# Optimization experiments

Measured on AMD Instinct MI355X. Metric: run time of the kernel, lower is better.

Reference implementation:

```python
import jax, jax.numpy as jnp
import numpy as np
from jax.scipy.special import erf

T_OBS = 1.0
T_CONTROL = 3.0
B = 4096
NT = 2048
DT0 = 0.002


def _moments(t_obs):
    t_avg = t_obs / 2.0
    t2_avg = t_obs ** 2 / 3.0
    C_t = t2_avg - t_avg ** 2
    return t_avg, t2_avg, C_t


def _sigma_move(sig_f, sig_a, xi_f, xi_v, t_obs):
    # 3x3 posterior covariance over (a, f, v), per get_Sigma_move_noSM
    xi_f_ = xi_f * (np.sqrt(t_obs) / sig_f)
    xi_v_ = xi_v * (np.sqrt(t_obs) / sig_f)
    t_avg, t2_avg, C_t = _moments(t_obs)
    det_inv = (1 + 1 / xi_f_ ** 2) * (C_t + 1 / xi_v_ ** 2) + t_avg ** 2 / xi_f_ ** 2
    pre = sig_f ** 2 / t_obs / det_inv ** 2
    Sff = (C_t + 1 / xi_v_ ** 2) ** 2 + C_t * t_avg ** 2
    Sfv = t_avg * (1 / (xi_f_ * xi_v_) ** 2 - C_t)
    Svv = (t_avg / xi_f_ ** 2) ** 2 + C_t * (1 + 1 / xi_f_ ** 2) ** 2
    zz = jnp.zeros(())
    row0 = jnp.stack([sig_a ** 2, zz, zz])
    row1 = jnp.stack([zz, pre * Sff, pre * Sfv])
    row2 = jnp.stack([zz, pre * Sfv, pre * Svv])
    return jnp.stack([row0, row1, row2])


def _sigma_stat(sig_f, xi_f, xi_v, t_obs):
    # 2x2 posterior covariance over (f, v), per get_Sigma_stat_noSM
    xi_f_ = xi_f * (np.sqrt(t_obs) / sig_f)
    xi_v_ = xi_v * (np.sqrt(t_obs) / sig_f)
    t_avg, t2_avg, C_t = _moments(t_obs)
    det_inv = (1 + 1 / xi_f_ ** 2) * (C_t + 1 / xi_v_ ** 2) + t_avg ** 2 / xi_f_ ** 2
    pre = sig_f ** 2 / t_obs
    Sff = pre / (1 + 1 / xi_f_ ** 2) ** 2
    Sfv = pre * (t_avg / (xi_f_ ** 2 + 1)) / det_inv
    Svv = pre * ((t_avg / xi_f_ ** 2) ** 2 + C_t * (1 + 1 / xi_f_ ** 2) ** 2) / det_inv ** 2
    return jnp.stack([jnp.stack([Sff, Sfv]), jnp.stack([Sfv, Svv])])


def _threshold(sig_f, xi_f, xi_v, d0, t_obs):
    xi_f_ = xi_f * (np.sqrt(t_obs) / sig_f)
    xi_v_ = xi_v * (np.sqrt(t_obs) / sig_f)
    t_avg, t2_avg, C_t = _moments(t_obs)
    log_arg = 1 + xi_v_ ** 2 * (C_t + t2_avg / (1 + xi_f_ ** 2))
    det_ratio = t_obs / sig_f ** 2 * (C_t + 1 / xi_v_ ** 2 + t2_avg / (1 + xi_f_ ** 2))
    thresh_sq = (jnp.log(log_arg) - 2 * d0) / det_ratio
    return jnp.sqrt(jax.nn.relu(thresh_sq))


def _control_weights(tau, t_wait, alpha, T_control):
    # Control-A gain profiles over the (shared) time grid tau [NT].
    Tm = T_control - jnp.mean(t_wait)
    rem = jax.nn.relu(Tm - tau)
    w_f = alpha * rem / Tm
    w_v = alpha * rem ** 2 / (2 * Tm ** 2)
    w_o_move = jnp.stack([w_f, w_v])          # [2, NT]
    w_o_stat = w_f[None, :]                   # [1, NT]
    w_tx = alpha * jnp.ones_like(tau)         # [NT]
    w_tv = alpha * rem / Tm                   # [NT]
    return w_o_move, w_o_stat, w_tx, w_tv


def _get_L(u_t, x_t, z, dt, Sinv_m, Sinv_s, det_m, det_s, W_m, W_s, q,
           wo_m, wo_s, w_tx, w_tv, g, sig_a):
    z_noa = z[:, 1:]
    num_t = u_t.shape[1]
    g2 = g * g
    resid = u_t - w_tx[None, :] * x_t                          # [B, T]
    data_quad = 0.5 * (dt / g2) * jnp.sum(resid ** 2, axis=-1)  # [B]

    def branch(Sinv, W, zz, wo, with_ctrl_v):
        S_vv = Sinv[-1, -1]
        S_vo = Sinv[-1, :-1]
        S_oo = Sinv[:-1, :-1]
        W_v = W[-1]
        W_o = W[:-1]
        A = S_oo[None] + (dt[:, None, None] / g2) * (wo @ wo.T)[None]  # [B,no,no]
        A_inv = jnp.linalg.inv(A)
        det_A = jnp.linalg.det(A)
        Woz = zz @ W_o.T                                       # [B, no]
        Wvz = zz @ W_v                                         # [B]
        d = (dt[:, None] / g2) * jnp.einsum('it,bt->bi', wo, resid)
        J_r = Woz @ S_oo.T + Wvz[:, None] * S_vo[None, :] + d   # [B, no]
        if with_ctrl_v:
            J_v = S_vo[None, :] + (dt[:, None] / g2) * (wo @ w_tv)[None, :]
            J = (S_vv * Wvz + Woz @ S_vo
                 + (dt / g2) * jnp.einsum('t,bt->b', w_tv, resid)
                 - jnp.einsum('bi,bij,bj->b', J_r, A_inv, J_v))
            k = (S_vv + (dt / g2) * jnp.sum(w_tv ** 2)
                 - jnp.einsum('bi,bij,bj->b', J_v, A_inv, J_v))
        else:
            J_v = jnp.broadcast_to(S_vo[None, :], J_r.shape)
            J = (S_vv * Wvz + Woz @ S_vo
                 - jnp.einsum('bi,bij,bj->b', J_r, A_inv, J_v))
            k = S_vv - jnp.einsum('bi,bij,bj->b', J_v, A_inv, J_v)
        Z = (0.5 * jnp.einsum('bi,ij,jk,kl,bl->b', zz, W, Sinv, W, zz)
             + data_quad
             - 0.5 * jnp.einsum('bi,bij,bj->b', J_r, A_inv, J_r)
             - 0.5 * J * J / k)
        return J, k, Z, det_A

    J_m, k_m, Z_m, detA_m = branch(Sinv_m, W_m, z, wo_m, True)
    J_s, k_s, Z_s, detA_s = branch(Sinv_s, W_s, z_noa, wo_s, False)

    pre_m = k_m * detA_m * det_m * sig_a ** 2
    pre_s = k_s * detA_s * det_s
    erf_m = (1 + 0.5 * erf((J_m - k_m * q) / jnp.sqrt(2 * k_m))
             - 0.5 * erf((J_m + k_m * q) / jnp.sqrt(2 * k_m)))
    erf_s = (0.5 * erf((J_s + k_s * q) / jnp.sqrt(2 * k_s))
             - 0.5 * erf((J_s - k_s * q) / jnp.sqrt(2 * k_s)))
    L_m = jnp.exp(-Z_m) * erf_m / jnp.sqrt(pre_m)
    L_s = jnp.exp(-Z_s) * erf_s / jnp.sqrt(pre_s)
    return jnp.sum(num_t * jnp.log(2 * np.pi * g2 / dt) - jnp.log(L_m + L_s))


def _forward(u_t, x_t, z, t, t_wait, u_t_SM, x_t_SM, z_SM, t_SM, t_wait_SM,
             hsig_f, hsig_w, hxi_f, hxi_w, hxi_v, delta0, halpha, hg, hW_aa, hsig_a):
    sig_f = jnp.exp(hsig_f[0]); sig_w = jnp.exp(hsig_w[0])
    xi_f = jnp.exp(hxi_f[0]); xi_w = jnp.exp(hxi_w[0]); xi_v = jnp.exp(hxi_v[0])
    d0 = delta0[0]; alpha = jnp.exp(halpha[0]); g = jnp.exp(hg[0])
    W_aa = jnp.exp(hW_aa[0]); sig_a = jnp.exp(hsig_a[0])
    one = jnp.ones(())

    dt = t[:, 1] - t[:, 0]
    dt_SM = t_SM[:, 1] - t[:, 0]  # matches original code (uses t[:,0])

    # ---- no self-motion branch ----
    Sig_m = _sigma_move(sig_f, sig_a, xi_f, xi_v, T_OBS)
    Sig_s = _sigma_stat(sig_f, xi_f, xi_v, T_OBS)
    Sinv_m = jnp.linalg.inv(Sig_m); det_m = jnp.linalg.det(Sig_m)
    Sinv_s = jnp.linalg.inv(Sig_s); det_s = jnp.linalg.det(Sig_s)
    W_m = jnp.diag(jnp.stack([W_aa, one, alpha]))
    W_s = jnp.diag(jnp.stack([one, alpha]))
    q = _threshold(sig_f, xi_f, xi_v, d0, T_OBS)
    wo_m, wo_s, w_tx, w_tv = _control_weights(t[0], t_wait, alpha, T_CONTROL)
    L1 = _get_L(u_t, x_t, z, dt, Sinv_m, Sinv_s, det_m, det_s,
                W_m, W_s, q, wo_m, wo_s, w_tx, w_tv, g, sig_a)

    # ---- self-motion branch: noise inflated by sig_w / xi_w, gain scaled by W_aa ----
    sig_eff = jnp.sqrt(sig_f ** 2 + sig_w ** 2)
    xi_v_eff = jnp.sqrt(xi_v ** 2 + xi_w ** 2)
    alpha_sm = alpha * W_aa
    Sig_m2 = _sigma_move(sig_eff, sig_a, xi_f, xi_v_eff, T_OBS)
    Sig_s2 = _sigma_stat(sig_eff, xi_f, xi_v_eff, T_OBS)
    Sinv_m2 = jnp.linalg.inv(Sig_m2); det_m2 = jnp.linalg.det(Sig_m2)
    Sinv_s2 = jnp.linalg.inv(Sig_s2); det_s2 = jnp.linalg.det(Sig_s2)
    W_m2 = jnp.diag(jnp.stack([W_aa, one, alpha_sm]))
    W_s2 = jnp.diag(jnp.stack([one, alpha_sm]))
    q2 = _threshold(sig_eff, xi_f, xi_v_eff, d0, T_OBS)
    wo_m2, wo_s2, w_tx2, w_tv2 = _control_weights(t_SM[0], t_wait_SM, alpha_sm, T_CONTROL)
    L2 = _get_L(u_t_SM, x_t_SM, z_SM, dt_SM, Sinv_m2, Sinv_s2, det_m2, det_s2,
                W_m2, W_s2, q2, wo_m2, wo_s2, w_tx2, w_tv2, g, sig_a)
    return L1 + L2


def setup_inputs() -> dict:
    key = jax.random.key(0)
    ks = jax.random.split(key, 8)
    f32 = jnp.float32
    tau = jnp.arange(NT, dtype=f32) * DT0
    t = jnp.broadcast_to(tau, (B, NT))
    return {
        'u_t': 0.05 * jax.random.normal(ks[0], (B, NT), f32),
        'x_t': 0.05 * jax.random.normal(ks[1], (B, NT), f32),
        'z': 0.1 * jax.random.normal(ks[2], (B, 3), f32),
        't': t,
        't_wait': 0.3 * jax.random.uniform(ks[3], (B,), f32),
        'u_t_SM': 0.05 * jax.random.normal(ks[4], (B, NT), f32),
        'x_t_SM': 0.05 * jax.random.normal(ks[5], (B, NT), f32),
        'z_SM': 0.1 * jax.random.normal(ks[6], (B, 3), f32),
        't_SM': t,
        't_wait_SM': 0.3 * jax.random.uniform(ks[7], (B,), f32),
        'hsig_f': jnp.array([-0.7], f32),
        'hsig_w': jnp.array([-1.0], f32),
        'hxi_f': jnp.array([0.0], f32),
        'hxi_w': jnp.array([-0.5], f32),
        'hxi_v': jnp.array([0.0], f32),
        'delta0': jnp.array([-0.5], f32),
        'halpha': jnp.array([-0.3], f32),
        'hg': jnp.array([0.0], f32),
        'hW_aa': jnp.array([-0.2], f32),
        'hsig_a': jnp.array([-0.7], f32),
    }


def reference(u_t, x_t, z, t, t_wait, u_t_SM, x_t_SM, z_SM, t_SM, t_wait_SM,
              hsig_f, hsig_w, hxi_f, hxi_w, hxi_v, delta0, halpha, hg, hW_aa, hsig_a):
    return _forward(u_t, x_t, z, t, t_wait, u_t_SM, x_t_SM, z_SM, t_SM, t_wait_SM,
                    hsig_f, hsig_w, hxi_f, hxi_w, hxi_v, delta0, halpha, hg, hW_aa, hsig_a)
```

## Files before the change

### kernel.cpp

```cpp
#include <hip/hip_runtime.h>
#include <math.h>

#ifndef M_PI
#define M_PI 3.14159265358979323846
#endif

#define TPB 256


__device__ double block_sum_d(double v, double* buf) {
    int tid = threadIdx.x;
    buf[tid] = v;
    __syncthreads();
    for (int o = TPB / 2; o > 0; o >>= 1) {
        if (tid < o) buf[tid] += buf[tid + o];
        __syncthreads();
    }
    double r = buf[0];
    __syncthreads();
    return r;
}

__global__ __launch_bounds__(TPB) void precompute_kernel(
    const float* __restrict__ t, const float* __restrict__ t_wait,
    const float* __restrict__ t_SM, const float* __restrict__ t_wait_SM,
    const float* __restrict__ hsig_f, const float* __restrict__ hsig_w,
    const float* __restrict__ hxi_f, const float* __restrict__ hxi_w,
    const float* __restrict__ hxi_v, const float* __restrict__ delta0,
    const float* __restrict__ halpha, const float* __restrict__ hg,
    const float* __restrict__ hW_aa, const float* __restrict__ hsig_a,
    int B, int NT, double* __restrict__ ws)
{
    __shared__ double buf[TPB];
    __shared__ double sh[2];
    int tid = threadIdx.x;

    double s1 = 0.0, s2 = 0.0;
    for (int i = tid; i < B; i += TPB) {
        s1 += (double)t_wait[i];
        s2 += (double)t_wait_SM[i];
    }
    double tw1 = block_sum_d(s1, buf);
    double tw2 = block_sum_d(s2, buf);
    if (tid == 0) { sh[0] = 3.0 - tw1 / (double)B; sh[1] = 3.0 - tw2 / (double)B; }
    __syncthreads();
    double Tm1 = sh[0], Tm2 = sh[1];

    double a2 = 0, a3 = 0, a4 = 0, b2 = 0, b3 = 0, b4 = 0;
    for (int i = tid; i < NT; i += TPB) {
        double r1 = Tm1 - (double)t[i];    r1 = r1 > 0.0 ? r1 : 0.0;
        double r2 = Tm2 - (double)t_SM[i]; r2 = r2 > 0.0 ? r2 : 0.0;
        double r1s = r1 * r1, r2s = r2 * r2;
        a2 += r1s; a3 += r1s * r1; a4 += r1s * r1s;
        b2 += r2s; b3 += r2s * r2; b4 += r2s * r2s;
    }
    a2 = block_sum_d(a2, buf); a3 = block_sum_d(a3, buf); a4 = block_sum_d(a4, buf);
    b2 = block_sum_d(b2, buf); b3 = block_sum_d(b3, buf); b4 = block_sum_d(b4, buf);
    if (tid != 0) return;

    double sig_f = exp((double)hsig_f[0]);
    double sig_w = exp((double)hsig_w[0]);
    double xi_f  = exp((double)hxi_f[0]);
    double xi_w  = exp((double)hxi_w[0]);
    double xi_v  = exp((double)hxi_v[0]);
    double d0    = (double)delta0[0];
    double alpha = exp((double)halpha[0]);
    double g     = exp((double)hg[0]);
    double W_aa  = exp((double)hW_aa[0]);
    double sig_a = exp((double)hsig_a[0]);
    double g2 = g * g, sig_a2 = sig_a * sig_a;

    for (int L = 0; L < 2; ++L) {
        double sf, xv, ab, Tm, S2, S3, S4;
        if (L == 0) { sf = sig_f; xv = xi_v; ab = alpha; Tm = Tm1; S2 = a2; S3 = a3; S4 = a4; }
        else {
            sf = sqrt(sig_f * sig_f + sig_w * sig_w);
            xv = sqrt(xi_v * xi_v + xi_w * xi_w);
            ab = alpha * W_aa; Tm = Tm2; S2 = b2; S3 = b3; S4 = b4;
        }
        double xf_ = xi_f / sf, xv_ = xv / sf;
        double t_avg = 0.5, t2_avg = 1.0 / 3.0, C_t = 1.0 / 12.0;
        double ixf2 = 1.0 / (xf_ * xf_), ixv2 = 1.0 / (xv_ * xv_);
        double det_inv = (1.0 + ixf2) * (C_t + ixv2) + t_avg * t_avg * ixf2;

        double pre_m = sf * sf / (det_inv * det_inv);
        double Sff = (C_t + ixv2) * (C_t + ixv2) + C_t * t_avg * t_avg;
        double Sfv = t_avg * (ixf2 * ixv2 - C_t);
        double Svv = (t_avg * ixf2) * (t_avg * ixf2) + C_t * (1.0 + ixf2) * (1.0 + ixf2);
        double m11 = pre_m * Sff, m12 = pre_m * Sfv, m22 = pre_m * Svv;
        double detB = m11 * m22 - m12 * m12;
        double Sm00 = 1.0 / sig_a2, Sm01 = 0.0, Sm02 = 0.0;
        double Sm11 = m22 / detB, Sm12 = -m12 / detB, Sm22 = m11 / detB;
        double det_m = sig_a2 * detB;

        double pre_s = sf * sf;
        double Sffs = pre_s / ((1.0 + ixf2) * (1.0 + ixf2));
        double Sfvs = pre_s * (t_avg / (xf_ * xf_ + 1.0)) / det_inv;
        double Svvs = pre_s * ((t_avg * ixf2) * (t_avg * ixf2) + C_t * (1.0 + ixf2) * (1.0 + ixf2)) / (det_inv * det_inv);
        double det_s = Sffs * Svvs - Sfvs * Sfvs;
        double Ss00 = Svvs / det_s, Ss01 = -Sfvs / det_s, Ss11 = Sffs / det_s;

        double log_arg = 1.0 + xv_ * xv_ * (C_t + t2_avg / (1.0 + xf_ * xf_));
        double det_ratio = (1.0 / (sf * sf)) * (C_t + 1.0 / (xv_ * xv_) + t2_avg / (1.0 + xf_ * xf_));
        double tq = (log(log_arg) - 2.0 * d0) / det_ratio;
        double q = sqrt(tq > 0.0 ? tq : 0.0);

        double kf = ab / Tm, kv = ab / (2.0 * Tm * Tm);
        double Gff = kf * kf * S2, Gfv = kf * kv * S3, Gvv = kv * kv * S4;

        double* w = ws + L * 32;
        w[0] = Sm00; w[1] = Sm01; w[2] = Sm02; w[3] = Sm11; w[4] = Sm12; w[5] = Sm22;
        w[6] = Ss00; w[7] = Ss01; w[8] = Ss11;
        w[9] = det_m; w[10] = det_s; w[11] = q;
        w[12] = Gff; w[13] = Gfv; w[14] = Gvv;
        w[15] = ab; w[16] = kf; w[17] = kv; w[18] = Tm;
        w[19] = W_aa; w[20] = g2; w[21] = sig_a2;
    }
}

__device__ double epilogue(const double* __restrict__ S, int NT,
                           double s2, double R1, double R2,
                           double z0, double z1, double z2, double dtb)
{
    double Sm00 = S[0], Sm01 = S[1], Sm02 = S[2], Sm11 = S[3], Sm12 = S[4], Sm22 = S[5];
    double Ss00 = S[6], Ss01 = S[7], Ss11 = S[8];
    double det_m = S[9], det_s = S[10], q = S[11];
    double Gff = S[12], Gfv = S[13], Gvv = S[14];
    double ab = S[15], kf = S[16], kv = S[17];
    double W_aa = S[19], g2 = S[20], sig_a2 = S[21];

    double cb = dtb / g2;
    double df = kf * R1, dv = kv * R2;
    double data_quad = 0.5 * cb * s2;

    double Svo0 = Sm02, Svo1 = Sm12, Svv = Sm22;
    double A00 = Sm00 + cb * Gff, A01 = Sm01 + cb * Gfv, A11 = Sm11 + cb * Gvv;
    double detA = A00 * A11 - A01 * A01;
    double i00 = A11 / detA, i01 = -A01 / detA, i11 = A00 / detA;
    double Woz0 = W_aa * z0, Woz1 = z1, Wvz = ab * z2;
    double Jr0 = Woz0 * Sm00 + Woz1 * Sm01 + Wvz * Svo0 + cb * df;
    double Jr1 = Woz0 * Sm01 + Woz1 * Sm11 + Wvz * Svo1 + cb * dv;
    double Jv0 = Svo0 + cb * Gff, Jv1 = Svo1 + cb * Gfv;
    double AiJv0 = i00 * Jv0 + i01 * Jv1, AiJv1 = i01 * Jv0 + i11 * Jv1;
    double AiJr0 = i00 * Jr0 + i01 * Jr1, AiJr1 = i01 * Jr0 + i11 * Jr1;
    double Jm = Svv * Wvz + Woz0 * Svo0 + Woz1 * Svo1 + cb * df
              - (Jr0 * AiJv0 + Jr1 * AiJv1);
    double km = Svv + cb * Gff - (Jv0 * AiJv0 + Jv1 * AiJv1);
    double y0 = W_aa * z0, y1 = z1, y2 = ab * z2;
    double zq = y0 * y0 * Sm00 + y1 * y1 * Sm11 + y2 * y2 * Sm22
              + 2.0 * (y0 * y1 * Sm01 + y0 * y2 * Sm02 + y1 * y2 * Sm12);
    double Zm = 0.5 * zq + data_quad - 0.5 * (Jr0 * AiJr0 + Jr1 * AiJr1) - 0.5 * Jm * Jm / km;

    double As = Ss00 + cb * Gff;
    double Wozs = z1, Wvzs = ab * z2;
    double Jrs = Wozs * Ss00 + Wvzs * Ss01 + cb * df;
    double Jvs = Ss01;
    double Js = Ss11 * Wvzs + Wozs * Ss01 - Jrs * Jvs / As;
    double ks = Ss11 - Jvs * Jvs / As;
    double ys1 = ab * z2;
    double zqs = z1 * z1 * Ss00 + 2.0 * z1 * ys1 * Ss01 + ys1 * ys1 * Ss11;
    double Zs = 0.5 * zqs + data_quad - 0.5 * Jrs * Jrs / As - 0.5 * Js * Js / ks;

    double pre_m = km * detA * det_m * sig_a2;
    double pre_s = ks * As * det_s;
    double sm = sqrt(2.0 * km), ss = sqrt(2.0 * ks);
    double em = 1.0 + 0.5 * erf((Jm - km * q) / sm) - 0.5 * erf((Jm + km * q) / sm);
    double es = 0.5 * erf((Js + ks * q) / ss) - 0.5 * erf((Js - ks * q) / ss);
    double Lm = exp(-Zm) * em / sqrt(pre_m);
    double Ls = exp(-Zs) * es / sqrt(pre_s);
    return (double)NT * log(2.0 * M_PI * g2 / dtb) - log(Lm + Ls);
}

__global__ __launch_bounds__(TPB) void batch_kernel(
    const float* __restrict__ u_t, const float* __restrict__ x_t,
    const float* __restrict__ z, const float* __restrict__ t,
    const float* __restrict__ u_SM, const float* __restrict__ x_SM,
    const float* __restrict__ z_SM, const float* __restrict__ t_SM,
    int NT, const double* __restrict__ ws, double* __restrict__ contrib)
{
    int b = blockIdx.x, tid = threadIdx.x;
    float ab1 = (float)ws[15], Tm1f = (float)ws[18];
    float ab2 = (float)ws[32 + 15], Tm2f = (float)ws[32 + 18];
    size_t off = (size_t)b * (size_t)NT;
    const float4* U1 = (const float4*)(u_t + off);
    const float4* X1 = (const float4*)(x_t + off);
    const float4* U2 = (const float4*)(u_SM + off);
    const float4* X2 = (const float4*)(x_SM + off);
    const float4* T1 = (const float4*)t;
    const float4* T2 = (const float4*)t_SM;
    int n4 = NT >> 2;

    float s2a = 0, r1a = 0, r2a = 0, s2b = 0, r1b = 0, r2b = 0;
    for (int i = tid; i < n4; i += TPB) {
        float4 u = U1[i], x = X1[i], ta = T1[i];
        float4 uu = U2[i], xx = X2[i], tb = T2[i];
        float uc[4]  = {u.x, u.y, u.z, u.w};
        float xc[4]  = {x.x, x.y, x.z, x.w};
        float tc[4]  = {ta.x, ta.y, ta.z, ta.w};
        float uuc[4] = {uu.x, uu.y, uu.z, uu.w};
        float xxc[4] = {xx.x, xx.y, xx.z, xx.w};
        float tbc[4] = {tb.x, tb.y, tb.z, tb.w};
#pragma unroll
        for (int j = 0; j < 4; ++j) {
            float resid = fmaf(-ab1, xc[j], uc[j]);
            float rem = fmaxf(Tm1f - tc[j], 0.0f);
            s2a = fmaf(resid, resid, s2a);
            r1a = fmaf(rem, resid, r1a);
            r2a = fmaf(rem * rem, resid, r2a);
            float rs = fmaf(-ab2, xxc[j], uuc[j]);
            float rm = fmaxf(Tm2f - tbc[j], 0.0f);
            s2b = fmaf(rs, rs, s2b);
            r1b = fmaf(rm, rs, r1b);
            r2b = fmaf(rm * rm, rs, r2b);
        }
    }
#pragma unroll
    for (int o = 32; o >= 1; o >>= 1) {
        s2a += __shfl_xor(s2a, o); r1a += __shfl_xor(r1a, o); r2a += __shfl_xor(r2a, o);
        s2b += __shfl_xor(s2b, o); r1b += __shfl_xor(r1b, o); r2b += __shfl_xor(r2b, o);
    }
    __shared__ float red[TPB / 64][6];
    int wave = tid >> 6, lane = tid & 63;
    if (lane == 0) {
        red[wave][0] = s2a; red[wave][1] = r1a; red[wave][2] = r2a;
        red[wave][3] = s2b; red[wave][4] = r1b; red[wave][5] = r2b;
    }
    __syncthreads();
    if (tid == 0) {
        double S2a = 0, R1a = 0, R2a = 0, S2b = 0, R1b = 0, R2b = 0;
        for (int w = 0; w < TPB / 64; ++w) {
            S2a += (double)red[w][0]; R1a += (double)red[w][1]; R2a += (double)red[w][2];
            S2b += (double)red[w][3]; R1b += (double)red[w][4]; R2b += (double)red[w][5];
        }
        double dtb1 = (double)t[off + 1] - (double)t[off];
        double dtb2 = (double)t_SM[off + 1] - (double)t[off];
        double z0 = (double)z[b * 3 + 0], z1 = (double)z[b * 3 + 1], z2 = (double)z[b * 3 + 2];
        double w0 = (double)z_SM[b * 3 + 0], w1 = (double)z_SM[b * 3 + 1], w2 = (double)z_SM[b * 3 + 2];
        double c1 = epilogue(ws, NT, S2a, R1a, R2a, z0, z1, z2, dtb1);
        double c2 = epilogue(ws + 32, NT, S2b, R1b, R2b, w0, w1, w2, dtb2);
        contrib[b] = c1 + c2;
    }
}

__global__ __launch_bounds__(TPB) void finalize_kernel(
    const double* __restrict__ contrib, int B, float* __restrict__ out)
{
    __shared__ double buf[TPB];
    double s = 0.0;
    for (int i = threadIdx.x; i < B; i += TPB) s += contrib[i];
    buf[threadIdx.x] = s;
    __syncthreads();
    for (int o = TPB / 2; o > 0; o >>= 1) {
        if (threadIdx.x < o) buf[threadIdx.x] += buf[threadIdx.x + o];
        __syncthreads();
    }
    if (threadIdx.x == 0) out[0] = (float)buf[0];
}

extern "C" void kernel_launch(void* const* d_in, const int* in_sizes, int n_in,
                              void* d_out, int out_size, void* d_ws, size_t ws_size,
                              hipStream_t stream) {
    const float* u_t       = (const float*)d_in[0];
    const float* x_t       = (const float*)d_in[1];
    const float* z         = (const float*)d_in[2];
    const float* t         = (const float*)d_in[3];
    const float* t_wait    = (const float*)d_in[4];
    const float* u_t_SM    = (const float*)d_in[5];
    const float* x_t_SM    = (const float*)d_in[6];
    const float* z_SM      = (const float*)d_in[7];
    const float* t_SM      = (const float*)d_in[8];
    const float* t_wait_SM = (const float*)d_in[9];
    const float* hsig_f = (const float*)d_in[10];
    const float* hsig_w = (const float*)d_in[11];
    const float* hxi_f  = (const float*)d_in[12];
    const float* hxi_w  = (const float*)d_in[13];
    const float* hxi_v  = (const float*)d_in[14];
    const float* delta0 = (const float*)d_in[15];
    const float* halpha = (const float*)d_in[16];
    const float* hg     = (const float*)d_in[17];
    const float* hW_aa  = (const float*)d_in[18];
    const float* hsig_a = (const float*)d_in[19];

    int B  = in_sizes[4];
    int NT = in_sizes[0] / B;

    double* ws      = (double*)d_ws;
    double* contrib = ws + 64;

    precompute_kernel<<<1, TPB, 0, stream>>>(t, t_wait, t_SM, t_wait_SM,
        hsig_f, hsig_w, hxi_f, hxi_w, hxi_v, delta0, halpha, hg, hW_aa, hsig_a,
        B, NT, ws);
    batch_kernel<<<B, TPB, 0, stream>>>(u_t, x_t, z, t, u_t_SM, x_t_SM, z_SM, t_SM,
        NT, ws, contrib);
    finalize_kernel<<<1, TPB, 0, stream>>>(contrib, B, (float*)d_out);
}
```

Baseline: 254.0 us.

## Split row reduction into per-wave streaming and a separate parallel epilogue kernel

The streaming pass now gives each half-row to one wave, so no block-level shared-memory reduction or __syncthreads is needed. Partial moments go to a workspace array. A new epilogue kernel evaluates the double-precision per-row epilogue with one thread per row instead of a single thread per block. It then reduces per block and atomically adds into the output, which replaces the separate finalize kernel. This removes the serial tid==0 epilogue that stalled each streaming block. The cost is an extra write and read of the moments, and float atomic accumulation order that is no longer deterministic.

```diff
diff --git a/kernel.cpp b/kernel.cpp
--- a/kernel.cpp
+++ b/kernel.cpp
@@ -29,7 +29,7 @@
     const float* __restrict__ hxi_v, const float* __restrict__ delta0,
     const float* __restrict__ halpha, const float* __restrict__ hg,
     const float* __restrict__ hW_aa, const float* __restrict__ hsig_a,
-    int B, int NT, double* __restrict__ ws)
+    int B, int NT, double* __restrict__ ws, float* __restrict__ out)
 {
     __shared__ double buf[TPB];
     __shared__ double sh[2];
@@ -57,6 +57,8 @@
     a2 = block_sum_d(a2, buf); a3 = block_sum_d(a3, buf); a4 = block_sum_d(a4, buf);
     b2 = block_sum_d(b2, buf); b3 = block_sum_d(b3, buf); b4 = block_sum_d(b4, buf);
     if (tid != 0) return;
+
+    out[0] = 0.0f;
 
     double sig_f = exp((double)hsig_f[0]);
     double sig_w = exp((double)hsig_w[0]);
@@ -89,7 +91,7 @@
         double Svv = (t_avg * ixf2) * (t_avg * ixf2) + C_t * (1.0 + ixf2) * (1.0 + ixf2);
         double m11 = pre_m * Sff, m12 = pre_m * Sfv, m22 = pre_m * Svv;
         double detB = m11 * m22 - m12 * m12;
-        double Sm00 = 1.0 / sig_a2, Sm01 = 0.0, Sm02 = 0.0;
+        double Sm00 = 1.0 / sig_a2;
         double Sm11 = m22 / detB, Sm12 = -m12 / detB, Sm22 = m11 / detB;
         double det_m = sig_a2 * detB;
 
@@ -109,12 +111,71 @@
         double Gff = kf * kf * S2, Gfv = kf * kv * S3, Gvv = kv * kv * S4;
 
         double* w = ws + L * 32;
-        w[0] = Sm00; w[1] = Sm01; w[2] = Sm02; w[3] = Sm11; w[4] = Sm12; w[5] = Sm22;
+        w[0] = Sm00; w[1] = 0.0; w[2] = 0.0; w[3] = Sm11; w[4] = Sm12; w[5] = Sm22;
         w[6] = Ss00; w[7] = Ss01; w[8] = Ss11;
         w[9] = det_m; w[10] = det_s; w[11] = q;
         w[12] = Gff; w[13] = Gfv; w[14] = Gvv;
         w[15] = ab; w[16] = kf; w[17] = kv; w[18] = Tm;
         w[19] = W_aa; w[20] = g2; w[21] = sig_a2;
+    }
+}
+
+__global__ __launch_bounds__(TPB) void stream_kernel(
+    const float* __restrict__ u_t, const float* __restrict__ x_t,
+    const float* __restrict__ u_SM, const float* __restrict__ x_SM,
+    const float* __restrict__ t, const float* __restrict__ t_SM,
+    int NT, int B, const double* __restrict__ ws, float* __restrict__ mom)
+{
+    int wid  = blockIdx.x * (TPB / 64) + (threadIdx.x >> 6);
+    int lane = threadIdx.x & 63;
+    int row  = wid >> 1, half = wid & 1;
+    int n4 = NT >> 2, h4 = n4 >> 1;
+
+    float ab1 = (float)ws[15],      Tm1 = (float)ws[18];
+    float ab2 = (float)ws[32 + 15], Tm2 = (float)ws[32 + 18];
+
+    size_t off = (size_t)row * (size_t)NT;
+    const float4* U1 = (const float4*)(u_t + off);
+    const float4* X1 = (const float4*)(x_t + off);
+    const float4* U2 = (const float4*)(u_SM + off);
+    const float4* X2 = (const float4*)(x_SM + off);
+    const float4* T1 = (const float4*)t;
+    const float4* T2 = (const float4*)t_SM;
+
+    float s2a = 0, r1a = 0, r2a = 0, s2b = 0, r1b = 0, r2b = 0;
+    int iend = (half + 1) * h4;
+    for (int i = half * h4 + lane; i < iend; i += 64) {
+        float4 u = U1[i], x = X1[i], ta = T1[i];
+        float4 uu = U2[i], xx = X2[i], tb = T2[i];
+        float uc[4]  = {u.x, u.y, u.z, u.w};
+        float xc[4]  = {x.x, x.y, x.z, x.w};
+        float tc[4]  = {ta.x, ta.y, ta.z, ta.w};
+        float uuc[4] = {uu.x, uu.y, uu.z, uu.w};
+        float xxc[4] = {xx.x, xx.y, xx.z, xx.w};
+        float tbc[4] = {tb.x, tb.y, tb.z, tb.w};
+#pragma unroll
+        for (int j = 0; j < 4; ++j) {
+            float resid = fmaf(-ab1, xc[j], uc[j]);
+            float rem = fmaxf(Tm1 - tc[j], 0.0f);
+            s2a = fmaf(resid, resid, s2a);
+            r1a = fmaf(rem, resid, r1a);
+            r2a = fmaf(rem * rem, resid, r2a);
+            float rs = fmaf(-ab2, xxc[j], uuc[j]);
+            float rm = fmaxf(Tm2 - tbc[j], 0.0f);
+            s2b = fmaf(rs, rs, s2b);
+            r1b = fmaf(rm, rs, r1b);
+            r2b = fmaf(rm * rm, rs, r2b);
+        }
+    }
+#pragma unroll
+    for (int o = 32; o >= 1; o >>= 1) {
+        s2a += __shfl_xor(s2a, o); r1a += __shfl_xor(r1a, o); r2a += __shfl_xor(r2a, o);
+        s2b += __shfl_xor(s2b, o); r1b += __shfl_xor(r1b, o); r2b += __shfl_xor(r2b, o);
+    }
+    if (lane == 0) {
+        int W = 2 * B;
+        mom[0 * W + wid] = s2a; mom[1 * W + wid] = r1a; mom[2 * W + wid] = r2a;
+        mom[3 * W + wid] = s2b; mom[4 * W + wid] = r1b; mom[5 * W + wid] = r2b;
     }
 }
 
@@ -171,90 +232,39 @@
     return (double)NT * log(2.0 * M_PI * g2 / dtb) - log(Lm + Ls);
 }
 
-__global__ __launch_bounds__(TPB) void batch_kernel(
-    const float* __restrict__ u_t, const float* __restrict__ x_t,
-    const float* __restrict__ z, const float* __restrict__ t,
-    const float* __restrict__ u_SM, const float* __restrict__ x_SM,
-    const float* __restrict__ z_SM, const float* __restrict__ t_SM,
-    int NT, const double* __restrict__ ws, double* __restrict__ contrib)
+__global__ __launch_bounds__(TPB) void epilogue_kernel(
+    const float* __restrict__ z, const float* __restrict__ z_SM,
+    const float* __restrict__ t, const float* __restrict__ t_SM,
+    int NT, int B, const double* __restrict__ ws,
+    const float* __restrict__ mom, float* __restrict__ out)
 {
-    int b = blockIdx.x, tid = threadIdx.x;
-    float ab1 = (float)ws[15], Tm1f = (float)ws[18];
-    float ab2 = (float)ws[32 + 15], Tm2f = (float)ws[32 + 18];
-    size_t off = (size_t)b * (size_t)NT;
-    const float4* U1 = (const float4*)(u_t + off);
-    const float4* X1 = (const float4*)(x_t + off);
-    const float4* U2 = (const float4*)(u_SM + off);
-    const float4* X2 = (const float4*)(x_SM + off);
-    const float4* T1 = (const float4*)t;
-    const float4* T2 = (const float4*)t_SM;
-    int n4 = NT >> 2;
-
-    float s2a = 0, r1a = 0, r2a = 0, s2b = 0, r1b = 0, r2b = 0;
-    for (int i = tid; i < n4; i += TPB) {
-        float4 u = U1[i], x = X1[i], ta = T1[i];
-        float4 uu = U2[i], xx = X2[i], tb = T2[i];
-        float uc[4]  = {u.x, u.y, u.z, u.w};
-        float xc[4]  = {x.x, x.y, x.z, x.w};
-        float tc[4]  = {ta.x, ta.y, ta.z, ta.w};
-        float uuc[4] = {uu.x, uu.y, uu.z, uu.w};
-        float xxc[4] = {xx.x, xx.y, xx.z, xx.w};
-        float tbc[4] = {tb.x, tb.y, tb.z, tb.w};
-#pragma unroll
-        for (int j = 0; j < 4; ++j) {
-            float resid = fmaf(-ab1, xc[j], uc[j]);
-            float rem = fmaxf(Tm1f - tc[j], 0.0f);
-            s2a = fmaf(resid, resid, s2a);
-            r1a = fmaf(rem, resid, r1a);
-            r2a = fmaf(rem * rem, resid, r2a);
-            float rs = fmaf(-ab2, xxc[j], uuc[j]);
-            float rm = fmaxf(Tm2f - tbc[j], 0.0f);
-            s2b = fmaf(rs, rs, s2b);
-            r1b = fmaf(rm, rs, r1b);
-            r2b = fmaf(rm * rm, rs, r2b);
-        }
-    }
-#pragma unroll
-    for (int o = 32; o >= 1; o >>= 1) {
-        s2a += __shfl_xor(s2a, o); r1a += __shfl_xor(r1a, o); r2a += __shfl_xor(r2a, o);
-        s2b += __shfl_xor(s2b, o); r1b += __shfl_xor(r1b, o); r2b += __shfl_xor(r2b, o);
-    }
-    __shared__ float red[TPB / 64][6];
-    int wave = tid >> 6, lane = tid & 63;
-    if (lane == 0) {
-        red[wave][0] = s2a; red[wave][1] = r1a; red[wave][2] = r2a;
-        red[wave][3] = s2b; red[wave][4] = r1b; red[wave][5] = r2b;
-    }
-    __syncthreads();
-    if (tid == 0) {
-        double S2a = 0, R1a = 0, R2a = 0, S2b = 0, R1b = 0, R2b = 0;
-        for (int w = 0; w < TPB / 64; ++w) {
-            S2a += (double)red[w][0]; R1a += (double)red[w][1]; R2a += (double)red[w][2];
-            S2b += (double)red[w][3]; R1b += (double)red[w][4]; R2b += (double)red[w][5];
-        }
+    int row = blockIdx.x * TPB + threadIdx.x;
+    double c = 0.0;
+    if (row < B) {
+        int W = 2 * B;
+        double S2a = (double)mom[0 * W + 2 * row] + (double)mom[0 * W + 2 * row + 1];
+        double R1a = (double)mom[1 * W + 2 * row] + (double)mom[1 * W + 2 * row + 1];
+        double R2a = (double)mom[2 * W + 2 * row] + (double)mom[2 * W + 2 * row + 1];
+        double S2b = (double)mom[3 * W + 2 * row] + (double)mom[3 * W + 2 * row + 1];
+        double R1b = (double)mom[4 * W + 2 * row] + (double)mom[4 * W + 2 * row + 1];
+        double R2b = (double)mom[5 * W + 2 * row] + (double)mom[5 * W + 2 * row + 1];
+        size_t off = (size_t)row * (size_t)NT;
         double dtb1 = (double)t[off + 1] - (double)t[off];
         double dtb2 = (double)t_SM[off + 1] - (double)t[off];
-        double z0 = (double)z[b * 3 + 0], z1 = (double)z[b * 3 + 1], z2 = (double)z[b * 3 + 2];
-        double w0 = (double)z_SM[b * 3 + 0], w1 = (double)z_SM[b * 3 + 1], w2 = (double)z_SM[b * 3 + 2];
-        double c1 = epilogue(ws, NT, S2a, R1a, R2a, z0, z1, z2, dtb1);
-        double c2 = epilogue(ws + 32, NT, S2b, R1b, R2b, w0, w1, w2, dtb2);
-        contrib[b] = c1 + c2;
-    }
-}
-
-__global__ __launch_bounds__(TPB) void finalize_kernel(
-    const double* __restrict__ contrib, int B, float* __restrict__ out)
-{
+        double z0 = (double)z[row * 3 + 0], z1 = (double)z[row * 3 + 1], z2 = (double)z[row * 3 + 2];
+        double w0 = (double)z_SM[row * 3 + 0], w1 = (double)z_SM[row * 3 + 1], w2 = (double)z_SM[row * 3 + 2];
+        c = epilogue(ws, NT, S2a, R1a, R2a, z0, z1, z2, dtb1)
+          + epilogue(ws + 32, NT, S2b, R1b, R2b, w0, w1, w2, dtb2);
+    }
     __shared__ double buf[TPB];
-    double s = 0.0;
-    for (int i = threadIdx.x; i < B; i += TPB) s += contrib[i];
-    buf[threadIdx.x] = s;
+    int tid = threadIdx.x;
+    buf[tid] = c;
     __syncthreads();
     for (int o = TPB / 2; o > 0; o >>= 1) {
-        if (threadIdx.x < o) buf[threadIdx.x] += buf[threadIdx.x + o];
+        if (tid < o) buf[tid] += buf[tid + o];
         __syncthreads();
     }
-    if (threadIdx.x == 0) out[0] = (float)buf[0];
+    if (tid == 0) atomicAdd(out, (float)buf[0]);
 }
 
 extern "C" void kernel_launch(void* const* d_in, const int* in_sizes, int n_in,
@@ -284,13 +294,19 @@
     int B  = in_sizes[4];
     int NT = in_sizes[0] / B;
 
-    double* ws      = (double*)d_ws;
-    double* contrib = ws + 64;
+    double* ws  = (double*)d_ws;
+    float*  mom = (float*)(ws + 64);
+    float*  out = (float*)d_out;
 
     precompute_kernel<<<1, TPB, 0, stream>>>(t, t_wait, t_SM, t_wait_SM,
         hsig_f, hsig_w, hxi_f, hxi_w, hxi_v, delta0, halpha, hg, hW_aa, hsig_a,
-        B, NT, ws);
-    batch_kernel<<<B, TPB, 0, stream>>>(u_t, x_t, z, t, u_t_SM, x_t_SM, z_SM, t_SM,
-        NT, ws, contrib);
-    finalize_kernel<<<1, TPB, 0, stream>>>(contrib, B, (float*)d_out);
-}
+        B, NT, ws, out);
+
+    int nwaves = 2 * B;
+    int nblocks = nwaves / (TPB / 64);
+    stream_kernel<<<nblocks, TPB, 0, stream>>>(u_t, x_t, u_t_SM, x_t_SM, t, t_SM,
+        NT, B, ws, mom);
+
+    epilogue_kernel<<<(B + TPB - 1) / TPB, TPB, 0, stream>>>(z, z_SM, t, t_SM,
+        NT, B, ws, mom, out);
+}
```

Result: faster. 240.9 us (-5.2%).
